# Kernel tuning notes

Hardware: AMD Instinct MI355X
Metric: run time of the kernel (lower is better)

## Reference

```python
import jax, jax.numpy as jnp
import numpy as np

B, L, E, H = 2, 4096, 1024, 16
D = E // H          # head_dim = 64
CHUNK = 256         # matches the torch module's chunk_size


def setup_inputs() -> dict:
    key = jax.random.key(0)
    k1, k2, k3 = jax.random.split(key, 3)
    x = jax.random.normal(k1, (B, L, E), dtype=jnp.float32)
    # torch Linear weight layout: (out_features, in_features); y = x @ W.T
    W_qkv = jax.random.normal(k2, (3 * E, E), dtype=jnp.float32) * 0.02
    W_out = jax.random.normal(k3, (E, E), dtype=jnp.float32) * 0.02
    return {"x": x, "W_qkv": W_qkv, "W_out": W_out}


def _linear_attention(x, W_qkv, W_out):
    Bz, Lz, Ez = x.shape
    scale = D ** (-0.5)
    qkv = x @ W_qkv.T                                # [B, L, 3E]
    qkv = qkv.reshape(Bz, Lz, 3, H, D).transpose(2, 0, 3, 1, 4)  # [3, B, H, L, D]
    q, k, v = qkv[0], qkv[1], qkv[2]
    # feature map: elu(x) + 1, query also scaled by head_dim^-0.5
    q = (jax.nn.elu(q) + 1.0) * scale
    k = jax.nn.elu(k) + 1.0

    nc = Lz // CHUNK  # seq_len chosen divisible by CHUNK
    def to_chunks(t):  # [B,H,L,D] -> [nc, B, H, CHUNK, D]
        return t.reshape(Bz, H, nc, CHUNK, D).transpose(2, 0, 1, 3, 4)
    qc, kc, vc = to_chunks(q), to_chunks(k), to_chunks(v)

    causal = jnp.tril(jnp.ones((CHUNK, CHUNK), dtype=x.dtype))

    def step(carry, inp):
        S, Z = carry                     # S: [B,H,D,D], Z: [B,H,D]
        qi, ki, vi = inp                 # each [B,H,CHUNK,D]
        # intra-chunk causal contribution (same math as cumsum of k v^T outer products)
        attn = jnp.einsum('bhld,bhmd->bhlm', qi, ki) * causal
        num = jnp.einsum('bhlm,bhme->bhle', attn, vi) + jnp.einsum('bhld,bhde->bhle', qi, S)
        den = attn.sum(-1) + jnp.einsum('bhld,bhd->bhl', qi, Z)
        S = S + jnp.einsum('bhmd,bhme->bhde', ki, vi)
        Z = Z + ki.sum(axis=2)
        return (S, Z), (num, den)

    S0 = jnp.zeros((Bz, H, D, D), dtype=x.dtype)
    Z0 = jnp.zeros((Bz, H, D), dtype=x.dtype)
    _, (num, den) = jax.lax.scan(step, (S0, Z0), (qc, kc, vc))
    # [nc,B,H,CHUNK,D] -> [B,H,L,D]
    num = num.transpose(1, 2, 0, 3, 4).reshape(Bz, H, Lz, D)
    den = den.transpose(1, 2, 0, 3).reshape(Bz, H, Lz)
    den = jnp.maximum(den, 1e-6)
    out = num / den[..., None]
    out = out.transpose(0, 2, 1, 3).reshape(Bz, Lz, Ez)
    return out @ W_out.T


def reference(x, W_qkv, W_out):
    return _linear_attention(x, W_qkv, W_out)
```

## Files before the change

### kernel.cpp

```cpp
#include <hip/hip_runtime.h>
#include <hip/hip_bf16.h>
#include <math.h>

#define B_ 2
#define L_ 4096
#define E_ 1024
#define H_ 16
#define D_ 64
#define CK_ 64
#define NC_ 64

typedef __bf16 bf16x8 __attribute__((ext_vector_type(8)));
typedef __bf16 bf16x4 __attribute__((ext_vector_type(4)));
typedef float  f32x4  __attribute__((ext_vector_type(4)));

__device__ __forceinline__ float fmap1(float x) { return x > 0.f ? x + 1.f : expf(x); }
__device__ __forceinline__ __bf16 f2b(float f) {
    __hip_bfloat16 h = __float2bfloat16(f); return *reinterpret_cast<__bf16*>(&h);
}
__device__ __forceinline__ unsigned short f2u(float f) {
    __hip_bfloat16 h = __float2bfloat16(f); return *reinterpret_cast<unsigned short*>(&h);
}

union U8 { bf16x8 v; __bf16 e[8]; bf16x4 half2[2]; };

__device__ __forceinline__ void async16(const __bf16* g, __bf16* lds) {
    __builtin_amdgcn_global_load_lds(
        (const __attribute__((address_space(1))) void*)g,
        (__attribute__((address_space(3))) void*)lds, 16, 0, 0);
}

__device__ __forceinline__ void flush_tile(const __bf16* rt, __hip_bfloat16* dst,
                                           size_t row_stride, int lane) {
    const int rr = lane >> 3, cc8 = (lane & 7) << 3;
#pragma unroll
    for (int p = 0; p < 8; ++p) {
        const int row = (p << 3) + rr;
        uint2 lo = *(const uint2*)&rt[row * 68 + cc8];
        uint2 hi = *(const uint2*)&rt[row * 68 + cc8 + 4];
        uint4 o = {lo.x, lo.y, hi.x, hi.y};
        *(uint4*)&dst[(size_t)row * row_stride + cc8] = o;
    }
}

__global__ __launch_bounds__(256) void cast_f32_bf16(const float* __restrict__ in,
                                                     __hip_bfloat16* __restrict__ out, int n) {
    int i = (blockIdx.x * 256 + threadIdx.x) << 2;
    if (i < n) {
        float4 v = *(const float4*)(in + i);
        ushort4 o = {f2u(v.x), f2u(v.y), f2u(v.z), f2u(v.w)};
        *(ushort4*)(out + i) = o;
    }
}

#define WVMC(n) do { asm volatile("s_waitcnt vmcnt(" #n ")" ::: "memory"); \
    __builtin_amdgcn_sched_barrier(0); } while (0)

template<int EPI>
__global__ __launch_bounds__(256) void gemm_mfma3(const __bf16* __restrict__ A,
                                                  const __bf16* __restrict__ Bw,
                                                  void* __restrict__ Cv,
                                                  __hip_bfloat16* __restrict__ KT,
                                                  __hip_bfloat16* __restrict__ VT,
                                                  int M, int N, int K) {
    __shared__ alignas(16) __bf16 As[3 * 4096];
    __shared__ alignas(16) __bf16 Bs[3 * 4096];
    const int tid = threadIdx.x;
    const int wave = tid >> 6, lane = tid & 63;
    const int wm = wave >> 1, wn = wave & 1;
    const int lq = lane >> 4, lr = lane & 15;

    const int nwg = gridDim.x * gridDim.y;
    const int bid = blockIdx.y * gridDim.x + blockIdx.x;
    const int cpx = nwg >> 3;
    const int wgid = (bid & 7) * cpx + (bid >> 3);
    const int bx = wgid % gridDim.x, by = wgid / gridDim.x;
    const int m0 = by * 128, n0 = bx * 128;

    const int NS = K >> 5;

    f32x4 acc[4][4];
#pragma unroll
    for (int i = 0; i < 4; ++i)
#pragma unroll
        for (int j = 0; j < 4; ++j) acc[i][j] = (f32x4){0.f, 0.f, 0.f, 0.f};

    const int stg_r = lane >> 2, stg_c = (lane & 3) << 3;
    const __bf16* Ag0 = A + (size_t)(m0 + (wave << 4) + stg_r) * K + stg_c;
    const __bf16* Ag1 = A + (size_t)(m0 + 64 + (wave << 4) + stg_r) * K + stg_c;
    const __bf16* Bg0 = Bw + (size_t)(n0 + (wave << 4) + stg_r) * K + stg_c;
    const __bf16* Bg1 = Bw + (size_t)(n0 + 64 + (wave << 4) + stg_r) * K + stg_c;
    const int dl0 = (wave << 9), dl1 = ((wave + 4) << 9);

#define STG3(bi, t) do { const int ko_ = (t) << 5; \
    async16(Ag0 + ko_, &As[(bi) * 4096 + dl0]); \
    async16(Ag1 + ko_, &As[(bi) * 4096 + dl1]); \
    async16(Bg0 + ko_, &Bs[(bi) * 4096 + dl0]); \
    async16(Bg1 + ko_, &Bs[(bi) * 4096 + dl1]); } while (0)

    STG3(0, 0);
    STG3(1, 1);
    WVMC(4);
    __builtin_amdgcn_s_barrier();

    int bi = 0, bn = 2;
    for (int t = 0; t < NS; ++t) {
        if (t + 2 < NS) STG3(bn, t + 2);
        bf16x8 af[4], bfr[4];
#pragma unroll
        for (int tt = 0; tt < 4; ++tt) {
            af[tt]  = *(const bf16x8*)&As[bi * 4096 + ((wm << 6) + (tt << 4) + lr) * 32 + (lq << 3)];
            bfr[tt] = *(const bf16x8*)&Bs[bi * 4096 + ((wn << 6) + (tt << 4) + lr) * 32 + (lq << 3)];
        }
#pragma unroll
        for (int mt = 0; mt < 4; ++mt)
#pragma unroll
            for (int nt = 0; nt < 4; ++nt)
                acc[mt][nt] = __builtin_amdgcn_mfma_f32_16x16x32_bf16(
                    af[mt], bfr[nt], acc[mt][nt], 0, 0, 0);
        if (t < NS - 2)       { WVMC(4); }
        else if (t == NS - 2) { WVMC(0); }
        __builtin_amdgcn_s_barrier();
        bi = (bi == 2) ? 0 : bi + 1;
        bn = (bn == 2) ? 0 : bn + 1;
    }

    const int M0 = m0 + (wm << 6);
    const int N0 = n0 + (wn << 6);
    if (EPI == 1) {
        __bf16* rt = ((wave & 2) ? Bs : As) + (wave & 1) * 4352;
        const int w = n0 >> 10;
        __hip_bfloat16* Cb = (__hip_bfloat16*)Cv;

        if (w <= 1) {
#pragma unroll
            for (int mt = 0; mt < 4; ++mt)
#pragma unroll
                for (int nt = 0; nt < 4; ++nt)
#pragma unroll
                    for (int r = 0; r < 4; ++r) {
                        float v = fmap1(acc[mt][nt][r]);
                        if (w == 0) v *= 0.125f;
                        rt[((mt << 4) + (lq << 2) + r) * 68 + (nt << 4) + lr] = f2b(v);
                    }
            flush_tile(rt, Cb + (size_t)M0 * N + N0, N, lane);
        }
        if (w >= 1) {
#pragma unroll
            for (int mt = 0; mt < 4; ++mt)
#pragma unroll
                for (int nt = 0; nt < 4; ++nt) {
                    ushort4 u;
                    if (w == 1)
                        u = (ushort4){f2u(fmap1(acc[mt][nt][0])), f2u(fmap1(acc[mt][nt][1])),
                                      f2u(fmap1(acc[mt][nt][2])), f2u(fmap1(acc[mt][nt][3]))};
                    else
                        u = (ushort4){f2u(acc[mt][nt][0]), f2u(acc[mt][nt][1]),
                                      f2u(acc[mt][nt][2]), f2u(acc[mt][nt][3])};
                    *(ushort4*)&rt[((nt << 4) + lr) * 68 + (mt << 4) + (lq << 2)] = u;
                }
            const int hh = (N0 >> 6) & 15;
            const int bb2 = M0 >> 12;
            const int l0 = M0 & 4095;
            __hip_bfloat16* T = (w == 1) ? KT : VT;
            flush_tile(rt, T + (((size_t)((bb2 * 16 + hh) << 6)) << 12) + l0, 4096, lane);
        }
    } else {
#pragma unroll
        for (int mt = 0; mt < 4; ++mt)
#pragma unroll
            for (int nt = 0; nt < 4; ++nt) {
                int m = M0 + (mt << 4) + (lq << 2);
                int n = N0 + (nt << 4) + lr;
#pragma unroll
                for (int r = 0; r < 4; ++r)
                    ((float*)Cv)[(size_t)(m + r) * N + n] = acc[mt][nt][r];
            }
    }
#undef STG3
}

__global__ __launch_bounds__(256) void chunk_state_mfma(const __hip_bfloat16* __restrict__ KTh,
                                                        const __hip_bfloat16* __restrict__ VTh,
                                                        __hip_bfloat16* __restrict__ Sb,
                                                        __hip_bfloat16* __restrict__ Zb) {
    __shared__ alignas(16) __bf16 rts[4][64 * 68];
    const int tid = threadIdx.x, wave = tid >> 6, lane = tid & 63;
    const int quad = lane >> 4, lr = lane & 15;
    const int bh = blockIdx.y;
    const int c = blockIdx.x * 4 + wave;
    const __bf16* KT = (const __bf16*)KTh;
    const __bf16* VT = (const __bf16*)VTh;
    __bf16* rt = rts[wave];

    bf16x8 vt[4][2], kt[4][2];
#pragma unroll
    for (int t = 0; t < 4; ++t)
#pragma unroll
        for (int kk = 0; kk < 2; ++kk) {
            size_t rowoff = ((size_t)(bh * 64 + t * 16 + lr) << 12) + c * CK_ + kk * 32 + quad * 8;
            vt[t][kk] = *(const bf16x8*)&VT[rowoff];
            kt[t][kk] = *(const bf16x8*)&KT[rowoff];
        }

    U8 of;
#pragma unroll
    for (int j = 0; j < 8; ++j) of.e[j] = f2b(1.0f);

#pragma unroll
    for (int es = 0; es < 4; ++es) {
#pragma unroll
        for (int dt = 0; dt < 4; ++dt) {
            f32x4 acc = (f32x4){0.f, 0.f, 0.f, 0.f};
            acc = __builtin_amdgcn_mfma_f32_16x16x32_bf16(vt[es][0], kt[dt][0], acc, 0, 0, 0);
            acc = __builtin_amdgcn_mfma_f32_16x16x32_bf16(vt[es][1], kt[dt][1], acc, 0, 0, 0);
#pragma unroll
            for (int r = 0; r < 4; ++r)
                rt[((es << 4) + (quad << 2) + r) * 68 + (dt << 4) + lr] = f2b(acc[r]);
        }
    }
    flush_tile(rt, Sb + ((size_t)(c * 32 + bh) << 12), 64, lane);

#pragma unroll
    for (int dt = 0; dt < 4; ++dt) {
        f32x4 z = (f32x4){0.f, 0.f, 0.f, 0.f};
        z = __builtin_amdgcn_mfma_f32_16x16x32_bf16(kt[dt][0], of.v, z, 0, 0, 0);
        z = __builtin_amdgcn_mfma_f32_16x16x32_bf16(kt[dt][1], of.v, z, 0, 0, 0);
        if (lr == 0) {
#pragma unroll
            for (int r = 0; r < 4; ++r)
                Zb[((c * 32 + bh) << 6) + dt * 16 + quad * 4 + r] = __float2bfloat16(z[r]);
        }
    }
}

__global__ __launch_bounds__(256) void prefix64(__hip_bfloat16* __restrict__ Sb,
                                                __hip_bfloat16* __restrict__ Zb) {
    const int bh = blockIdx.y;
    const int idx = blockIdx.x * 256 + threadIdx.x;
    float v[NC_];
#pragma unroll
    for (int c = 0; c < NC_; ++c)
        v[c] = __bfloat162float(Sb[((size_t)(c * 32 + bh) << 12) + idx]);
    float run = 0.f;
#pragma unroll
    for (int c = 0; c < NC_; ++c) {
        Sb[((size_t)(c * 32 + bh) << 12) + idx] = __float2bfloat16(run);
        run += v[c];
    }
    if (blockIdx.x == 0 && threadIdx.x < 64) {
        float z[NC_];
#pragma unroll
        for (int c = 0; c < NC_; ++c)
            z[c] = __bfloat162float(Zb[((c * 32 + bh) << 6) + threadIdx.x]);
        float zr = 0.f;
#pragma unroll
        for (int c = 0; c < NC_; ++c) {
            Zb[((c * 32 + bh) << 6) + threadIdx.x] = __float2bfloat16(zr);
            zr += z[c];
        }
    }
}

__global__ __launch_bounds__(256) void attn_out_mfma(const __hip_bfloat16* __restrict__ qvh,
                                                     const __hip_bfloat16* __restrict__ Sbh,
                                                     const __hip_bfloat16* __restrict__ Zbh,
                                                     const __hip_bfloat16* __restrict__ VTh,
                                                     __hip_bfloat16* __restrict__ attn) {
    __shared__ __bf16 Pbuf[4 * 64 * 68];
    const int tid = threadIdx.x, wave = tid >> 6, lane = tid & 63;
    const int quad = lane >> 4, lr = lane & 15;
    const int bh = blockIdx.y, b = bh >> 4, h = bh & 15;
    const int c = blockIdx.x * 4 + wave;
    const size_t t0 = (size_t)b * L_ + c * CK_;
    const __bf16* qb = (const __bf16*)qvh;
    const __bf16* Sb = (const __bf16*)Sbh;
    const __bf16* Zb = (const __bf16*)Zbh;
    const __bf16* VT = (const __bf16*)VTh;
    __bf16* P = Pbuf + wave * (64 * 68);

    bf16x8 qf[4][2];
#pragma unroll
    for (int ls = 0; ls < 4; ++ls)
#pragma unroll
        for (int kk = 0; kk < 2; ++kk)
            qf[ls][kk] = *(const bf16x8*)&qb[(t0 + ls * 16 + lr) * 3072 + h * 64 + kk * 32 + quad * 8];

    f32x4 num[4][4], den[4];
#pragma unroll
    for (int i = 0; i < 4; ++i) {
        den[i] = (f32x4){0.f, 0.f, 0.f, 0.f};
#pragma unroll
        for (int j = 0; j < 4; ++j) num[i][j] = (f32x4){0.f, 0.f, 0.f, 0.f};
    }

    bf16x8 zf[2];
#pragma unroll
    for (int kk = 0; kk < 2; ++kk)
        zf[kk] = *(const bf16x8*)&Zb[((size_t)(c * 32 + bh) << 6) + kk * 32 + quad * 8];
#pragma unroll
    for (int ls = 0; ls < 4; ++ls)
#pragma unroll
        for (int kk = 0; kk < 2; ++kk)
            den[ls] = __builtin_amdgcn_mfma_f32_16x16x32_bf16(qf[ls][kk], zf[kk], den[ls], 0, 0, 0);

#pragma unroll
    for (int es = 0; es < 4; ++es) {
        bf16x8 sf[2];
#pragma unroll
        for (int kk = 0; kk < 2; ++kk)
            sf[kk] = *(const bf16x8*)&Sb[((size_t)(c * 32 + bh) << 12)
                                         + (es * 16 + lr) * 64 + kk * 32 + quad * 8];
#pragma unroll
        for (int ls = 0; ls < 4; ++ls)
#pragma unroll
            for (int kk = 0; kk < 2; ++kk)
                num[ls][es] = __builtin_amdgcn_mfma_f32_16x16x32_bf16(
                    qf[ls][kk], sf[kk], num[ls][es], 0, 0, 0);
    }

    bf16x8 kf[4][2];
#pragma unroll
    for (int ms = 0; ms < 4; ++ms)
#pragma unroll
        for (int kk = 0; kk < 2; ++kk)
            kf[ms][kk] = *(const bf16x8*)&qb[(t0 + ms * 16 + lr) * 3072 + 1024 + h * 64 + kk * 32 + quad * 8];

#pragma unroll
    for (int ls = 0; ls < 4; ++ls) {
#pragma unroll
        for (int ms = 0; ms < 4; ++ms) {
            int off = (ls * 16 + lr) * 68 + ms * 16 + quad * 4;
            if (ms <= ls) {
                f32x4 pt = (f32x4){0.f, 0.f, 0.f, 0.f};
                pt = __builtin_amdgcn_mfma_f32_16x16x32_bf16(kf[ms][0], qf[ls][0], pt, 0, 0, 0);
                pt = __builtin_amdgcn_mfma_f32_16x16x32_bf16(kf[ms][1], qf[ls][1], pt, 0, 0, 0);
                ushort4 u;
                if (ms == ls) {
                    u.x = (quad * 4 + 0 > lr) ? 0 : f2u(pt[0]);
                    u.y = (quad * 4 + 1 > lr) ? 0 : f2u(pt[1]);
                    u.z = (quad * 4 + 2 > lr) ? 0 : f2u(pt[2]);
                    u.w = (quad * 4 + 3 > lr) ? 0 : f2u(pt[3]);
                } else {
                    u = (ushort4){f2u(pt[0]), f2u(pt[1]), f2u(pt[2]), f2u(pt[3])};
                }
                *(ushort4*)&P[off] = u;
            } else {
                *(ushort4*)&P[off] = (ushort4){0, 0, 0, 0};
            }
        }
    }

    U8 of;
#pragma unroll
    for (int j = 0; j < 8; ++j) of.e[j] = f2b(1.0f);

#pragma unroll
    for (int kk = 0; kk < 2; ++kk) {
        U8 pf[4];
#pragma unroll
        for (int ls = 0; ls < 4; ++ls) {
            pf[ls].half2[0] = *(const bf16x4*)&P[(ls * 16 + lr) * 68 + kk * 32 + quad * 8];
            pf[ls].half2[1] = *(const bf16x4*)&P[(ls * 16 + lr) * 68 + kk * 32 + quad * 8 + 4];
        }
        bf16x8 vf[4];
#pragma unroll
        for (int es = 0; es < 4; ++es)
            vf[es] = *(const bf16x8*)&VT[((size_t)((b * 16 + h) * 64 + es * 16 + lr) << 12)
                                         + c * CK_ + kk * 32 + quad * 8];
#pragma unroll
        for (int ls = 0; ls < 4; ++ls) {
            den[ls] = __builtin_amdgcn_mfma_f32_16x16x32_bf16(pf[ls].v, of.v, den[ls], 0, 0, 0);
#pragma unroll
            for (int es = 0; es < 4; ++es)
                num[ls][es] = __builtin_amdgcn_mfma_f32_16x16x32_bf16(
                    pf[ls].v, vf[es], num[ls][es], 0, 0, 0);
        }
    }

#pragma unroll
    for (int ls = 0; ls < 4; ++ls)
#pragma unroll
        for (int r = 0; r < 4; ++r) {
            float inv = 1.f / fmaxf(den[ls][r], 1e-6f);
#pragma unroll
            for (int es = 0; es < 4; ++es)
                P[((ls << 4) + (quad << 2) + r) * 68 + (es << 4) + lr] =
                    f2b(num[ls][es][r] * inv);
        }
    flush_tile(P, attn + t0 * 1024 + (h << 6), 1024, lane);
}

extern "C" void kernel_launch(void* const* d_in, const int* in_sizes, int n_in,
                              void* d_out, int out_size, void* d_ws, size_t ws_size,
                              hipStream_t stream) {
    (void)ws_size; (void)out_size;
    const float *x = nullptr, *Wqkv = nullptr, *Wout = nullptr;
    for (int i = 0; i < n_in; ++i) {
        if (in_sizes[i] == 8388608)      x    = (const float*)d_in[i];
        else if (in_sizes[i] == 3145728) Wqkv = (const float*)d_in[i];
        else if (in_sizes[i] == 1048576) Wout = (const float*)d_in[i];
    }

    __hip_bfloat16* ws16  = (__hip_bfloat16*)d_ws;
    __hip_bfloat16* xb    = ws16;
    __hip_bfloat16* attn  = ws16;
    __hip_bfloat16* Wqkvb = ws16 + 8388608;
    __hip_bfloat16* Woutb = Wqkvb + 3145728;
    __hip_bfloat16* qv    = Woutb + 1048576;
    __hip_bfloat16* VT    = qv + 25165824;
    __hip_bfloat16* KT    = VT + 8388608;
    __hip_bfloat16* Sb    = KT + 8388608;
    __hip_bfloat16* Zb    = Sb + 8388608;

    cast_f32_bf16<<<8388608 / 1024, 256, 0, stream>>>(x, xb, 8388608);
    cast_f32_bf16<<<3145728 / 1024, 256, 0, stream>>>(Wqkv, Wqkvb, 3145728);
    cast_f32_bf16<<<1048576 / 1024, 256, 0, stream>>>(Wout, Woutb, 1048576);

    gemm_mfma3<1><<<dim3(3072 / 128, 8192 / 128), 256, 0, stream>>>(
        (const __bf16*)xb, (const __bf16*)Wqkvb, qv, KT, VT, B_ * L_, 3 * E_, E_);
    chunk_state_mfma<<<dim3(16, B_ * H_), 256, 0, stream>>>(KT, VT, Sb, Zb);
    prefix64<<<dim3(16, B_ * H_), 256, 0, stream>>>(Sb, Zb);
    attn_out_mfma<<<dim3(16, B_ * H_), 256, 0, stream>>>(qv, Sb, Zb, VT, attn);
    gemm_mfma3<0><<<dim3(1024 / 128, 8192 / 128), 256, 0, stream>>>(
        (const __bf16*)attn, (const __bf16*)Woutb, d_out, nullptr, nullptr, B_ * L_, E_, E_);
}
```

Baseline: 230.8 us.

## Split each chunk across two waves in chunk-state and attention-output kernels

The chunk-state and attention-output kernels used to assign one 64-token chunk to each wave. They now assign one chunk per 128-thread block and split the value-dimension tiles between the two waves. In attention output, each wave computes half of the causal QK^T tile into shared LDS, and the waves synchronise before the P·V and output write. This doubles wave-level parallelism per chunk, which should shorten per-wave latency in these small grids. In exchange it adds barriers, duplicates the Q loads and the denominator work in both waves, and launches more, smaller blocks.

```diff
diff --git a/kernel.cpp b/kernel.cpp
--- a/kernel.cpp
+++ b/kernel.cpp
@@ -35,6 +35,18 @@
     const int rr = lane >> 3, cc8 = (lane & 7) << 3;
 #pragma unroll
     for (int p = 0; p < 8; ++p) {
+        const int row = (p << 3) + rr;
+        uint2 lo = *(const uint2*)&rt[row * 68 + cc8];
+        uint2 hi = *(const uint2*)&rt[row * 68 + cc8 + 4];
+        uint4 o = {lo.x, lo.y, hi.x, hi.y};
+        *(uint4*)&dst[(size_t)row * row_stride + cc8] = o;
+    }
+}
+__device__ __forceinline__ void flush32x64(const __bf16* rt, __hip_bfloat16* dst,
+                                           size_t row_stride, int lane) {
+    const int rr = lane >> 3, cc8 = (lane & 7) << 3;
+#pragma unroll
+    for (int p = 0; p < 4; ++p) {
         const int row = (p << 3) + rr;
         uint2 lo = *(const uint2*)&rt[row * 68 + cc8];
         uint2 hi = *(const uint2*)&rt[row * 68 + cc8 + 4];
@@ -180,56 +192,61 @@
 #undef STG3
 }
 
-__global__ __launch_bounds__(256) void chunk_state_mfma(const __hip_bfloat16* __restrict__ KTh,
-                                                        const __hip_bfloat16* __restrict__ VTh,
-                                                        __hip_bfloat16* __restrict__ Sb,
-                                                        __hip_bfloat16* __restrict__ Zb) {
-    __shared__ alignas(16) __bf16 rts[4][64 * 68];
+__global__ __launch_bounds__(128) void chunk_state_split(const __hip_bfloat16* __restrict__ KTh,
+                                                         const __hip_bfloat16* __restrict__ VTh,
+                                                         __hip_bfloat16* __restrict__ Sb,
+                                                         __hip_bfloat16* __restrict__ Zb) {
+    __shared__ alignas(16) __bf16 rts[2][32 * 68];
     const int tid = threadIdx.x, wave = tid >> 6, lane = tid & 63;
     const int quad = lane >> 4, lr = lane & 15;
     const int bh = blockIdx.y;
-    const int c = blockIdx.x * 4 + wave;
+    const int c = blockIdx.x;
     const __bf16* KT = (const __bf16*)KTh;
     const __bf16* VT = (const __bf16*)VTh;
     __bf16* rt = rts[wave];
 
-    bf16x8 vt[4][2], kt[4][2];
-#pragma unroll
-    for (int t = 0; t < 4; ++t)
-#pragma unroll
-        for (int kk = 0; kk < 2; ++kk) {
-            size_t rowoff = ((size_t)(bh * 64 + t * 16 + lr) << 12) + c * CK_ + kk * 32 + quad * 8;
-            vt[t][kk] = *(const bf16x8*)&VT[rowoff];
-            kt[t][kk] = *(const bf16x8*)&KT[rowoff];
-        }
-
-    U8 of;
-#pragma unroll
-    for (int j = 0; j < 8; ++j) of.e[j] = f2b(1.0f);
-
-#pragma unroll
-    for (int es = 0; es < 4; ++es) {
+    bf16x8 kt[4][2], vt2[2][2];
+#pragma unroll
+    for (int dt = 0; dt < 4; ++dt)
+#pragma unroll
+        for (int kk = 0; kk < 2; ++kk)
+            kt[dt][kk] = *(const bf16x8*)&KT[((size_t)(bh * 64 + dt * 16 + lr) << 12)
+                                             + c * CK_ + kk * 32 + quad * 8];
+#pragma unroll
+    for (int esl = 0; esl < 2; ++esl)
+#pragma unroll
+        for (int kk = 0; kk < 2; ++kk)
+            vt2[esl][kk] = *(const bf16x8*)&VT[((size_t)(bh * 64 + (wave * 2 + esl) * 16 + lr) << 12)
+                                               + c * CK_ + kk * 32 + quad * 8];
+
+#pragma unroll
+    for (int esl = 0; esl < 2; ++esl) {
 #pragma unroll
         for (int dt = 0; dt < 4; ++dt) {
             f32x4 acc = (f32x4){0.f, 0.f, 0.f, 0.f};
-            acc = __builtin_amdgcn_mfma_f32_16x16x32_bf16(vt[es][0], kt[dt][0], acc, 0, 0, 0);
-            acc = __builtin_amdgcn_mfma_f32_16x16x32_bf16(vt[es][1], kt[dt][1], acc, 0, 0, 0);
+            acc = __builtin_amdgcn_mfma_f32_16x16x32_bf16(vt2[esl][0], kt[dt][0], acc, 0, 0, 0);
+            acc = __builtin_amdgcn_mfma_f32_16x16x32_bf16(vt2[esl][1], kt[dt][1], acc, 0, 0, 0);
 #pragma unroll
             for (int r = 0; r < 4; ++r)
-                rt[((es << 4) + (quad << 2) + r) * 68 + (dt << 4) + lr] = f2b(acc[r]);
-        }
-    }
-    flush_tile(rt, Sb + ((size_t)(c * 32 + bh) << 12), 64, lane);
-
-#pragma unroll
-    for (int dt = 0; dt < 4; ++dt) {
-        f32x4 z = (f32x4){0.f, 0.f, 0.f, 0.f};
-        z = __builtin_amdgcn_mfma_f32_16x16x32_bf16(kt[dt][0], of.v, z, 0, 0, 0);
-        z = __builtin_amdgcn_mfma_f32_16x16x32_bf16(kt[dt][1], of.v, z, 0, 0, 0);
-        if (lr == 0) {
-#pragma unroll
-            for (int r = 0; r < 4; ++r)
-                Zb[((c * 32 + bh) << 6) + dt * 16 + quad * 4 + r] = __float2bfloat16(z[r]);
+                rt[((esl << 4) + (quad << 2) + r) * 68 + (dt << 4) + lr] = f2b(acc[r]);
+        }
+    }
+    flush32x64(rt, Sb + ((size_t)(c * 32 + bh) << 12) + (size_t)(wave * 32) * 64, 64, lane);
+
+    if (wave == 0) {
+        U8 of;
+#pragma unroll
+        for (int j = 0; j < 8; ++j) of.e[j] = f2b(1.0f);
+#pragma unroll
+        for (int dt = 0; dt < 4; ++dt) {
+            f32x4 z = (f32x4){0.f, 0.f, 0.f, 0.f};
+            z = __builtin_amdgcn_mfma_f32_16x16x32_bf16(kt[dt][0], of.v, z, 0, 0, 0);
+            z = __builtin_amdgcn_mfma_f32_16x16x32_bf16(kt[dt][1], of.v, z, 0, 0, 0);
+            if (lr == 0) {
+#pragma unroll
+                for (int r = 0; r < 4; ++r)
+                    Zb[((c * 32 + bh) << 6) + dt * 16 + quad * 4 + r] = __float2bfloat16(z[r]);
+            }
         }
     }
 }
@@ -262,22 +279,21 @@
     }
 }
 
-__global__ __launch_bounds__(256) void attn_out_mfma(const __hip_bfloat16* __restrict__ qvh,
-                                                     const __hip_bfloat16* __restrict__ Sbh,
-                                                     const __hip_bfloat16* __restrict__ Zbh,
-                                                     const __hip_bfloat16* __restrict__ VTh,
-                                                     __hip_bfloat16* __restrict__ attn) {
-    __shared__ __bf16 Pbuf[4 * 64 * 68];
+__global__ __launch_bounds__(128) void attn_out_split(const __hip_bfloat16* __restrict__ qvh,
+                                                      const __hip_bfloat16* __restrict__ Sbh,
+                                                      const __hip_bfloat16* __restrict__ Zbh,
+                                                      const __hip_bfloat16* __restrict__ VTh,
+                                                      __hip_bfloat16* __restrict__ attn) {
+    __shared__ alignas(16) __bf16 P[64 * 68];
     const int tid = threadIdx.x, wave = tid >> 6, lane = tid & 63;
     const int quad = lane >> 4, lr = lane & 15;
     const int bh = blockIdx.y, b = bh >> 4, h = bh & 15;
-    const int c = blockIdx.x * 4 + wave;
+    const int c = blockIdx.x;
     const size_t t0 = (size_t)b * L_ + c * CK_;
     const __bf16* qb = (const __bf16*)qvh;
     const __bf16* Sb = (const __bf16*)Sbh;
     const __bf16* Zb = (const __bf16*)Zbh;
     const __bf16* VT = (const __bf16*)VTh;
-    __bf16* P = Pbuf + wave * (64 * 68);
 
     bf16x8 qf[4][2];
 #pragma unroll
@@ -286,14 +302,48 @@
         for (int kk = 0; kk < 2; ++kk)
             qf[ls][kk] = *(const bf16x8*)&qb[(t0 + ls * 16 + lr) * 3072 + h * 64 + kk * 32 + quad * 8];
 
-    f32x4 num[4][4], den[4];
+    const int msA = wave ? 1 : 0;
+    const int msB = wave ? 2 : 3;
+    bf16x8 kfA[2], kfB[2];
+#pragma unroll
+    for (int kk = 0; kk < 2; ++kk) {
+        kfA[kk] = *(const bf16x8*)&qb[(t0 + msA * 16 + lr) * 3072 + 1024 + h * 64 + kk * 32 + quad * 8];
+        kfB[kk] = *(const bf16x8*)&qb[(t0 + msB * 16 + lr) * 3072 + 1024 + h * 64 + kk * 32 + quad * 8];
+    }
+#define PT_MS(kf_, ms_) \
+    _Pragma("unroll") for (int ls = 0; ls < 4; ++ls) { \
+        const int off_ = (ls * 16 + lr) * 68 + (ms_) * 16 + quad * 4; \
+        if ((ms_) <= ls) { \
+            f32x4 pt = (f32x4){0.f, 0.f, 0.f, 0.f}; \
+            pt = __builtin_amdgcn_mfma_f32_16x16x32_bf16(kf_[0], qf[ls][0], pt, 0, 0, 0); \
+            pt = __builtin_amdgcn_mfma_f32_16x16x32_bf16(kf_[1], qf[ls][1], pt, 0, 0, 0); \
+            ushort4 u; \
+            if ((ms_) == ls) { \
+                u.x = (quad * 4 + 0 > lr) ? 0 : f2u(pt[0]); \
+                u.y = (quad * 4 + 1 > lr) ? 0 : f2u(pt[1]); \
+                u.z = (quad * 4 + 2 > lr) ? 0 : f2u(pt[2]); \
+                u.w = (quad * 4 + 3 > lr) ? 0 : f2u(pt[3]); \
+            } else { \
+                u = (ushort4){f2u(pt[0]), f2u(pt[1]), f2u(pt[2]), f2u(pt[3])}; \
+            } \
+            *(ushort4*)&P[off_] = u; \
+        } else { \
+            *(ushort4*)&P[off_] = (ushort4){0, 0, 0, 0}; \
+        } \
+    }
+    PT_MS(kfA, msA);
+    PT_MS(kfB, msB);
+#undef PT_MS
+    __syncthreads();
+
+    const int es0 = wave << 1;
+    f32x4 num[4][2], den[4];
 #pragma unroll
     for (int i = 0; i < 4; ++i) {
         den[i] = (f32x4){0.f, 0.f, 0.f, 0.f};
-#pragma unroll
-        for (int j = 0; j < 4; ++j) num[i][j] = (f32x4){0.f, 0.f, 0.f, 0.f};
-    }
-
+        num[i][0] = (f32x4){0.f, 0.f, 0.f, 0.f};
+        num[i][1] = (f32x4){0.f, 0.f, 0.f, 0.f};
+    }
     bf16x8 zf[2];
 #pragma unroll
     for (int kk = 0; kk < 2; ++kk)
@@ -303,58 +353,24 @@
 #pragma unroll
         for (int kk = 0; kk < 2; ++kk)
             den[ls] = __builtin_amdgcn_mfma_f32_16x16x32_bf16(qf[ls][kk], zf[kk], den[ls], 0, 0, 0);
-
-#pragma unroll
-    for (int es = 0; es < 4; ++es) {
+#pragma unroll
+    for (int esl = 0; esl < 2; ++esl) {
         bf16x8 sf[2];
 #pragma unroll
         for (int kk = 0; kk < 2; ++kk)
             sf[kk] = *(const bf16x8*)&Sb[((size_t)(c * 32 + bh) << 12)
-                                         + (es * 16 + lr) * 64 + kk * 32 + quad * 8];
+                                         + ((es0 + esl) * 16 + lr) * 64 + kk * 32 + quad * 8];
 #pragma unroll
         for (int ls = 0; ls < 4; ++ls)
 #pragma unroll
             for (int kk = 0; kk < 2; ++kk)
-                num[ls][es] = __builtin_amdgcn_mfma_f32_16x16x32_bf16(
-                    qf[ls][kk], sf[kk], num[ls][es], 0, 0, 0);
-    }
-
-    bf16x8 kf[4][2];
-#pragma unroll
-    for (int ms = 0; ms < 4; ++ms)
-#pragma unroll
-        for (int kk = 0; kk < 2; ++kk)
-            kf[ms][kk] = *(const bf16x8*)&qb[(t0 + ms * 16 + lr) * 3072 + 1024 + h * 64 + kk * 32 + quad * 8];
-
-#pragma unroll
-    for (int ls = 0; ls < 4; ++ls) {
-#pragma unroll
-        for (int ms = 0; ms < 4; ++ms) {
-            int off = (ls * 16 + lr) * 68 + ms * 16 + quad * 4;
-            if (ms <= ls) {
-                f32x4 pt = (f32x4){0.f, 0.f, 0.f, 0.f};
-                pt = __builtin_amdgcn_mfma_f32_16x16x32_bf16(kf[ms][0], qf[ls][0], pt, 0, 0, 0);
-                pt = __builtin_amdgcn_mfma_f32_16x16x32_bf16(kf[ms][1], qf[ls][1], pt, 0, 0, 0);
-                ushort4 u;
-                if (ms == ls) {
-                    u.x = (quad * 4 + 0 > lr) ? 0 : f2u(pt[0]);
-                    u.y = (quad * 4 + 1 > lr) ? 0 : f2u(pt[1]);
-                    u.z = (quad * 4 + 2 > lr) ? 0 : f2u(pt[2]);
-                    u.w = (quad * 4 + 3 > lr) ? 0 : f2u(pt[3]);
-                } else {
-                    u = (ushort4){f2u(pt[0]), f2u(pt[1]), f2u(pt[2]), f2u(pt[3])};
-                }
-                *(ushort4*)&P[off] = u;
-            } else {
-                *(ushort4*)&P[off] = (ushort4){0, 0, 0, 0};
-            }
-        }
+                num[ls][esl] = __builtin_amdgcn_mfma_f32_16x16x32_bf16(
+                    qf[ls][kk], sf[kk], num[ls][esl], 0, 0, 0);
     }
 
     U8 of;
 #pragma unroll
     for (int j = 0; j < 8; ++j) of.e[j] = f2b(1.0f);
-
 #pragma unroll
     for (int kk = 0; kk < 2; ++kk) {
         U8 pf[4];
@@ -363,32 +379,45 @@
             pf[ls].half2[0] = *(const bf16x4*)&P[(ls * 16 + lr) * 68 + kk * 32 + quad * 8];
             pf[ls].half2[1] = *(const bf16x4*)&P[(ls * 16 + lr) * 68 + kk * 32 + quad * 8 + 4];
         }
-        bf16x8 vf[4];
-#pragma unroll
-        for (int es = 0; es < 4; ++es)
-            vf[es] = *(const bf16x8*)&VT[((size_t)((b * 16 + h) * 64 + es * 16 + lr) << 12)
-                                         + c * CK_ + kk * 32 + quad * 8];
+        bf16x8 vf[2];
+#pragma unroll
+        for (int esl = 0; esl < 2; ++esl)
+            vf[esl] = *(const bf16x8*)&VT[((size_t)((b * 16 + h) * 64 + (es0 + esl) * 16 + lr) << 12)
+                                          + c * CK_ + kk * 32 + quad * 8];
 #pragma unroll
         for (int ls = 0; ls < 4; ++ls) {
             den[ls] = __builtin_amdgcn_mfma_f32_16x16x32_bf16(pf[ls].v, of.v, den[ls], 0, 0, 0);
 #pragma unroll
-            for (int es = 0; es < 4; ++es)
-                num[ls][es] = __builtin_amdgcn_mfma_f32_16x16x32_bf16(
-                    pf[ls].v, vf[es], num[ls][es], 0, 0, 0);
-        }
-    }
-
+            for (int esl = 0; esl < 2; ++esl)
+                num[ls][esl] = __builtin_amdgcn_mfma_f32_16x16x32_bf16(
+                    pf[ls].v, vf[esl], num[ls][esl], 0, 0, 0);
+        }
+    }
+
+    __syncthreads();
 #pragma unroll
     for (int ls = 0; ls < 4; ++ls)
 #pragma unroll
         for (int r = 0; r < 4; ++r) {
             float inv = 1.f / fmaxf(den[ls][r], 1e-6f);
 #pragma unroll
-            for (int es = 0; es < 4; ++es)
-                P[((ls << 4) + (quad << 2) + r) * 68 + (es << 4) + lr] =
-                    f2b(num[ls][es][r] * inv);
-        }
-    flush_tile(P, attn + t0 * 1024 + (h << 6), 1024, lane);
+            for (int esl = 0; esl < 2; ++esl)
+                P[((ls << 4) + (quad << 2) + r) * 68 + ((es0 + esl) << 4) + lr] =
+                    f2b(num[ls][esl][r] * inv);
+        }
+    __syncthreads();
+    {
+        const int rr = tid >> 3, cc8 = (tid & 7) << 3;
+        __hip_bfloat16* dst = attn + t0 * 1024 + (h << 6);
+#pragma unroll
+        for (int p = 0; p < 4; ++p) {
+            const int row = (p << 4) + rr;
+            uint2 lo = *(const uint2*)&P[row * 68 + cc8];
+            uint2 hi = *(const uint2*)&P[row * 68 + cc8 + 4];
+            uint4 o = {lo.x, lo.y, hi.x, hi.y};
+            *(uint4*)&dst[(size_t)row * 1024 + cc8] = o;
+        }
+    }
 }
 
 extern "C" void kernel_launch(void* const* d_in, const int* in_sizes, int n_in,
@@ -419,9 +448,9 @@
 
     gemm_mfma3<1><<<dim3(3072 / 128, 8192 / 128), 256, 0, stream>>>(
         (const __bf16*)xb, (const __bf16*)Wqkvb, qv, KT, VT, B_ * L_, 3 * E_, E_);
-    chunk_state_mfma<<<dim3(16, B_ * H_), 256, 0, stream>>>(KT, VT, Sb, Zb);
+    chunk_state_split<<<dim3(64, B_ * H_), 128, 0, stream>>>(KT, VT, Sb, Zb);
     prefix64<<<dim3(16, B_ * H_), 256, 0, stream>>>(Sb, Zb);
-    attn_out_mfma<<<dim3(16, B_ * H_), 256, 0, stream>>>(qv, Sb, Zb, VT, attn);
+    attn_out_split<<<dim3(64, B_ * H_), 128, 0, stream>>>(qv, Sb, Zb, VT, attn);
     gemm_mfma3<0><<<dim3(1024 / 128, 8192 / 128), 256, 0, stream>>>(
         (const __bf16*)attn, (const __bf16*)Woutb, d_out, nullptr, nullptr, B_ * L_, E_, E_);
 }
```

Result: no change. 235.0 us (+1.9%).
